# Optimization experiments

Measured on AMD Instinct MI355X. Metric: run time of the kernel, lower is better.

The kernel has to match this reference:

```python
import jax, jax.numpy as jnp
import numpy as np

INHIBITION = 3.0

def kwta(x, gates):
    # per-row k = argmax index of the gate row; keep the top-k values of x,
    # damp all other entries by 1/INHIBITION (matches torch loop + topk + scatter)
    k = jnp.argmax(gates, axis=1)                          # [B] int
    ranks = jnp.argsort(jnp.argsort(-x, axis=1), axis=1)   # rank 0 == largest
    keep = ranks < k[:, None]
    return jnp.where(keep, x, x / INHIBITION)

def _linear_init(key, out_d, in_d):
    k1, k2 = jax.random.split(key)
    lim = 1.0 / np.sqrt(in_d)
    W = jax.random.uniform(k1, (out_d, in_d), jnp.float32, -lim, lim)
    b = jax.random.uniform(k2, (out_d,), jnp.float32, -lim, lim)
    return W, b

def setup_inputs() -> dict:
    key = jax.random.key(0)
    B, S, H, HID = 16384, 512, 256, 512
    inp_dim = 2 * S + 4 + H  # 1284
    keys = jax.random.split(key, 13)
    d = {}
    d["state"] = jax.random.normal(keys[0], (B, 2 * S), jnp.float32)
    d["task_indicator"] = jax.random.normal(keys[1], (B, 4), jnp.float32)
    d["action"] = jax.random.normal(keys[2], (B, H), jnp.float32)
    specs = [("cx1_1", 2 * HID, inp_dim), ("cx1_2", 2 * HID, 2 * HID),
             ("cx2_1", HID, inp_dim), ("cx2_2", HID, HID),
             ("cx3_1", H, inp_dim), ("cx3_2", H, H),
             ("l1", 2 * HID, inp_dim), ("l2", HID, 2 * HID),
             ("l3", H, HID), ("l4", H, H)]
    for i, (name, o, idim) in enumerate(specs):
        W, b = _linear_init(keys[3 + i], o, idim)
        d["W_" + name] = W
        d["b_" + name] = b
    return d

def reference(state, task_indicator, action,
              W_cx1_1, b_cx1_1, W_cx1_2, b_cx1_2,
              W_cx2_1, b_cx2_1, W_cx2_2, b_cx2_2,
              W_cx3_1, b_cx3_1, W_cx3_2, b_cx3_2,
              W_l1, b_l1, W_l2, b_l2, W_l3, b_l3, W_l4, b_l4):
    ctx = jnp.concatenate([state, task_indicator, action], axis=1)  # [B, 1284]

    def gate(Wa, ba, Wb, bb):
        h = jnp.tanh(ctx @ Wa.T + ba)
        return jax.nn.softmax(h @ Wb.T + bb, axis=1)

    cx1 = gate(W_cx1_1, b_cx1_1, W_cx1_2, b_cx1_2)  # [B, 1024]
    cx2 = gate(W_cx2_1, b_cx2_1, W_cx2_2, b_cx2_2)  # [B, 512]
    cx3 = gate(W_cx3_1, b_cx3_1, W_cx3_2, b_cx3_2)  # [B, 256]

    x = kwta(ctx @ W_l1.T + b_l1, cx1)
    x = kwta(x @ W_l2.T + b_l2, cx2)
    x = kwta(x @ W_l3.T + b_l3, cx3)
    return x @ W_l4.T + b_l4  # [B, 256]
```

## Files before the change

kernel.cpp:

```cpp
#include <hip/hip_runtime.h>
#include <math.h>

typedef float  v4f   __attribute__((ext_vector_type(4)));
typedef double v2d   __attribute__((ext_vector_type(2)));
typedef double v4d   __attribute__((ext_vector_type(4)));
typedef float  f32x4 __attribute__((ext_vector_type(4)));
typedef short  s16x8 __attribute__((ext_vector_type(8)));

#define NB   16384
#define KCTX 1284
#define CSL  (KCTX/4)

#if defined(__has_builtin)
#  if __has_builtin(__builtin_amdgcn_mfma_f64_16x16x4f64)
#    define MFMA64(a, b, c) __builtin_amdgcn_mfma_f64_16x16x4f64((a), (b), (c), 0, 0, 0)
#  endif
#endif
#ifndef MFMA64
static __device__ __forceinline__ v4d mfma64_asm(double a, double b, v4d c) {
  asm volatile("v_mfma_f64_16x16x4_f64 %0, %1, %2, %0" : "+v"(c) : "v"(a), "v"(b));
  return c;
}
#  define MFMA64(a, b, c) mfma64_asm((a), (b), (c))
#endif

static __device__ __forceinline__ f32x4 mfma_bf16(s16x8 a, s16x8 b, f32x4 c) {
  asm volatile("v_mfma_f32_16x16x32_bf16 %0, %1, %2, %0" : "+v"(c) : "v"(a), "v"(b));
  return c;
}
#define MFMA_GUARD() do {                                  \
  __builtin_amdgcn_sched_barrier(0);                       \
  asm volatile("s_nop 7\ns_nop 7\ns_nop 7\ns_nop 7");      \
  __builtin_amdgcn_sched_barrier(0);                       \
} while (0)

__global__ __launch_bounds__(256) void k_build_ctx(
    const float* __restrict__ state, const float* __restrict__ task,
    const float* __restrict__ action, float* __restrict__ Cg)
{
  int idx = blockIdx.x * 256 + threadIdx.x;
  if (idx >= NB * CSL) return;
  int b = idx / CSL, s = idx - b * CSL;
  v4f v;
  if (s < 256)       v = *((const v4f*)state  + (size_t)b * 256 + s);
  else if (s == 256) v = *((const v4f*)task   + b);
  else               v = *((const v4f*)action + (size_t)b * 64 + (s - 257));
  *((v4f*)Cg + idx) = v;
}

__device__ __forceinline__ unsigned long long f64_ord(double f) {
  unsigned long long u = (unsigned long long)__double_as_longlong(f);
  return (u & 0x8000000000000000ull) ? ~u : (u | 0x8000000000000000ull);
}

__global__ __launch_bounds__(256) void k_split_w(
    const float* __restrict__ W, unsigned short* __restrict__ out,
    int N, int K, int KP)
{
  int idx = blockIdx.x * 256 + threadIdx.x;
  size_t total = (size_t)N * KP;
  if (idx >= (int)total) return;
  int n = idx / KP, k = idx - n * KP;
  float v = (k < K) ? W[(size_t)n * K + k] : 0.f;
  unsigned u1 = __float_as_uint(v);
  float f1 = __uint_as_float(u1 & 0xFFFF0000u);
  float r1 = v - f1;
  unsigned u2 = __float_as_uint(r1);
  float f2 = __uint_as_float(u2 & 0xFFFF0000u);
  float r2 = r1 - f2;
  out[idx]             = (unsigned short)(u1 >> 16);
  out[total + idx]     = (unsigned short)(u2 >> 16);
  out[2 * total + idx] = (unsigned short)(__float_as_uint(r2) >> 16);
}

#define TM 128
#define TN 64
#define TK 16
#define LRA 130
#define LRB 66

template<int EPI, int ASRC>
__global__ __launch_bounds__(256, 3) void g64m(
    const void* __restrict__ Av, const float* __restrict__ W,
    const float* __restrict__ bias, void* __restrict__ Cv,
    unsigned long long* __restrict__ kpk, int N, int K)
{
  __shared__ __align__(16) double As[TK * LRA];
  __shared__ __align__(16) double Ws[TK * LRB];

  const int tid  = threadIdx.x;
  const int lane = tid & 63;
  const int wid  = tid >> 6;
  const int wm   = wid >> 1;
  const int wn   = wid & 1;
  const int grp  = lane >> 4;
  const int lid  = lane & 15;
  const int row0 = blockIdx.x * TM;
  const int col0 = blockIdx.y * TN;

  const int lrA = tid >> 1;
  const int lcA = (tid & 1) * 8;
  const int lrW = tid >> 2;
  const int lcW = (tid & 3) * 4;

  const float*  ApF = (const float*)Av  + (size_t)(row0 + lrA) * K;
  const double* ApD = (const double*)Av + (size_t)(row0 + lrA) * K;
  const float*  WpF = W + (size_t)(col0 + lrW) * K;

  double sa[8], sw[4];

  v4d acc[4][2];
  #pragma unroll
  for (int i = 0; i < 4; ++i)
    #pragma unroll
    for (int j = 0; j < 2; ++j) { acc[i][j][0] = 0.0; acc[i][j][1] = 0.0;
                                  acc[i][j][2] = 0.0; acc[i][j][3] = 0.0; }

  const int nt = (K + TK - 1) / TK;

  auto loadA = [&](int k0) {
    const int kb = k0 + lcA;
    if (ASRC == 0) {
      if (kb + 8 <= K) {
        v4f x0 = *(const v4f*)(ApF + kb), x1 = *(const v4f*)(ApF + kb + 4);
        sa[0] = x0.x; sa[1] = x0.y; sa[2] = x0.z; sa[3] = x0.w;
        sa[4] = x1.x; sa[5] = x1.y; sa[6] = x1.z; sa[7] = x1.w;
      } else {
        #pragma unroll
        for (int j = 0; j < 8; ++j) sa[j] = (kb + j < K) ? (double)ApF[kb + j] : 0.0;
      }
    } else {
      const double* p = ApD + kb;
      v2d d0 = *(const v2d*)p,       d1 = *(const v2d*)(p + 2);
      v2d d2 = *(const v2d*)(p + 4), d3 = *(const v2d*)(p + 6);
      sa[0] = d0.x; sa[1] = d0.y; sa[2] = d1.x; sa[3] = d1.y;
      sa[4] = d2.x; sa[5] = d2.y; sa[6] = d3.x; sa[7] = d3.y;
    }
  };
  auto loadW = [&](int k0) {
    const int kb = k0 + lcW;
    if (kb + 4 <= K) {
      v4f w0 = *(const v4f*)(WpF + kb);
      sw[0] = w0.x; sw[1] = w0.y; sw[2] = w0.z; sw[3] = w0.w;
    } else {
      #pragma unroll
      for (int j = 0; j < 4; ++j) sw[j] = (kb + j < K) ? (double)WpF[kb + j] : 0.0;
    }
  };

  loadA(0); loadW(0);

  for (int t = 0; t < nt; ++t) {
    __syncthreads();
    #pragma unroll
    for (int j = 0; j < 8; ++j) As[(lcA + j) * LRA + lrA] = sa[j];
    #pragma unroll
    for (int j = 0; j < 4; ++j) Ws[(lcW + j) * LRB + lrW] = sw[j];
    if (t + 1 < nt) { loadA((t + 1) * TK); loadW((t + 1) * TK); }
    __syncthreads();
    #pragma unroll
    for (int ks = 0; ks < 4; ++ks) {
      const double* Ar = As + (ks * 4 + grp) * LRA + wm * 64 + lid;
      const double* Br = Ws + (ks * 4 + grp) * LRB + wn * 32 + lid;
      double a[4], b[2];
      #pragma unroll
      for (int i = 0; i < 4; ++i) a[i] = Ar[i * 16];
      #pragma unroll
      for (int j = 0; j < 2; ++j) b[j] = Br[j * 16];
      #pragma unroll
      for (int i = 0; i < 4; ++i)
        #pragma unroll
        for (int j = 0; j < 2; ++j)
          acc[i][j] = MFMA64(a[i], b[j], acc[i][j]);
    }
  }

  double bb[2];
  #pragma unroll
  for (int j = 0; j < 2; ++j) bb[j] = (double)bias[col0 + wn * 32 + j * 16 + lid];

  if (EPI == 0) {
    #pragma unroll
    for (int i = 0; i < 4; ++i)
      #pragma unroll
      for (int r = 0; r < 4; ++r) {
        int row = row0 + wm * 64 + i * 16 + r * 4 + grp;
        double* Cp = (double*)Cv + (size_t)row * N + col0 + wn * 32 + lid;
        #pragma unroll
        for (int j = 0; j < 2; ++j) Cp[j * 16] = acc[i][j][r] + bb[j];
      }
  } else if (EPI == 3 || EPI == 4) {
    #pragma unroll
    for (int i = 0; i < 4; ++i)
      #pragma unroll
      for (int r = 0; r < 4; ++r) {
        int row = row0 + wm * 64 + i * 16 + r * 4 + grp;
        float* Cp = (float*)Cv + (size_t)row * N + col0 + wn * 32 + lid;
        #pragma unroll
        for (int j = 0; j < 2; ++j) {
          double o = acc[i][j][r] + bb[j];
          if (EPI == 4) o = tanh(o);
          Cp[j * 16] = (float)o;
        }
      }
  } else {
    #pragma unroll
    for (int i = 0; i < 4; ++i)
      #pragma unroll
      for (int r = 0; r < 4; ++r) {
        int row = row0 + wm * 64 + i * 16 + r * 4 + grp;
        double best = acc[i][0][r] + bb[0];
        int bcol = col0 + wn * 32 + lid;
        {
          double v = acc[i][1][r] + bb[1];
          if (v > best) { best = v; bcol = col0 + wn * 32 + 16 + lid; }
        }
        #pragma unroll
        for (int d = 1; d < 16; d <<= 1) {
          double ov = __shfl_xor(best, d);
          int    oc = __shfl_xor(bcol, d);
          if (ov > best || (ov == best && oc < bcol)) { best = ov; bcol = oc; }
        }
        if (lid == 0) {
          unsigned long long key =
              (f64_ord(best) & ~0xFFFFull) | ((~(unsigned)bcol) & 0xFFFFu);
          atomicMax(&kpk[row], key);
        }
      }
  }
}

#define GTM 64
#define GTN 128
#define GTK 32
#define GLR 40

template<int EPI, int ASPLIT>
__global__ __launch_bounds__(256, 2) void g16(
    const void* __restrict__ Av, size_t aplane,
    const unsigned short* __restrict__ WS_,
    const float* __restrict__ bias,
    unsigned short* __restrict__ Hout, size_t hplane,
    unsigned long long* __restrict__ kpk, int N, int K, int KP)
{
  __shared__ __align__(16) unsigned short Al[3][GTM * GLR];
  __shared__ __align__(16) unsigned short Wl[3][GTN * GLR];

  const int tid  = threadIdx.x;
  const int lane = tid & 63;
  const int wid  = tid >> 6;
  const int grp  = lane >> 4;
  const int lid  = lane & 15;
  const int row0 = blockIdx.x * GTM;
  const int col0 = blockIdx.y * GTN;

  const int arow = tid >> 2, akc = (tid & 3) * 8;
  const int wrow = tid >> 1, wkc = (tid & 1) * 16;
  const float*          ApF = (const float*)Av + (size_t)(row0 + arow) * K;
  const unsigned short* ApS = (const unsigned short*)Av + (size_t)(row0 + arow) * K;
  const unsigned short* WpS = WS_ + (size_t)(col0 + wrow) * KP + wkc;
  const size_t wplane = (size_t)N * KP;

  float av[8];
  s16x8 sA[3], sW[3][2];

  f32x4 ah[4][2], am[4][2], al[4][2];
  double sh[4][2][4];
  #pragma unroll
  for (int i = 0; i < 4; ++i)
    #pragma unroll
    for (int j = 0; j < 2; ++j) {
      ah[i][j] = (f32x4)0.f; am[i][j] = (f32x4)0.f; al[i][j] = (f32x4)0.f;
      #pragma unroll
      for (int r = 0; r < 4; ++r) sh[i][j][r] = 0.0;
    }

  const int nt = KP / GTK;

  auto loadA = [&](int kb) {
    if (ASPLIT == 0) {
      #pragma unroll
      for (int q = 0; q < 2; ++q) {
        int k = kb + akc + q * 4;
        if (k + 4 <= K) {
          v4f x = *(const v4f*)(ApF + k);
          av[q*4+0] = x.x; av[q*4+1] = x.y; av[q*4+2] = x.z; av[q*4+3] = x.w;
        } else {
          #pragma unroll
          for (int j = 0; j < 4; ++j) av[q*4+j] = (k + j < K) ? ApF[k + j] : 0.f;
        }
      }
    } else {
      #pragma unroll
      for (int p = 0; p < 3; ++p)
        sA[p] = *(const s16x8*)(ApS + p * aplane + kb + akc);
    }
  };
  auto loadW = [&](int kb) {
    #pragma unroll
    for (int p = 0; p < 3; ++p) {
      const unsigned short* s = WpS + p * wplane + kb;
      sW[p][0] = *(const s16x8*)s;
      sW[p][1] = *(const s16x8*)(s + 8);
    }
  };

  auto split8 = [](const float* v, s16x8& p1, s16x8& p2, s16x8& p3) {
    #pragma unroll
    for (int j = 0; j < 8; ++j) {
      unsigned u1 = __float_as_uint(v[j]);
      float f1 = __uint_as_float(u1 & 0xFFFF0000u);
      float r1 = v[j] - f1;
      unsigned u2 = __float_as_uint(r1);
      float f2 = __uint_as_float(u2 & 0xFFFF0000u);
      float r2 = r1 - f2;
      p1[j] = (short)(u1 >> 16); p2[j] = (short)(u2 >> 16);
      p3[j] = (short)(__float_as_uint(r2) >> 16);
    }
  };

  loadA(0); loadW(0);

  for (int t = 0; t < nt; ++t) {
    __syncthreads();
    if (ASPLIT == 0) {
      s16x8 p1, p2, p3;
      split8(av, p1, p2, p3);
      *(s16x8*)&Al[0][arow * GLR + akc] = p1;
      *(s16x8*)&Al[1][arow * GLR + akc] = p2;
      *(s16x8*)&Al[2][arow * GLR + akc] = p3;
    } else {
      #pragma unroll
      for (int p = 0; p < 3; ++p)
        *(s16x8*)&Al[p][arow * GLR + akc] = sA[p];
    }
    #pragma unroll
    for (int p = 0; p < 3; ++p) {
      *(s16x8*)&Wl[p][wrow * GLR + wkc]     = sW[p][0];
      *(s16x8*)&Wl[p][wrow * GLR + wkc + 8] = sW[p][1];
    }
    if (t + 1 < nt) { loadA((t + 1) * GTK); loadW((t + 1) * GTK); }
    __syncthreads();

    s16x8 b0[2], b1[2], b2[2];
    #pragma unroll
    for (int nf = 0; nf < 2; ++nf) {
      int widx = (wid * 32 + nf * 16 + lid) * GLR + grp * 8;
      b0[nf] = *(const s16x8*)&Wl[0][widx];
      b1[nf] = *(const s16x8*)&Wl[1][widx];
      b2[nf] = *(const s16x8*)&Wl[2][widx];
    }
    #pragma unroll
    for (int mf = 0; mf < 4; ++mf) {
      int aidx = (mf * 16 + lid) * GLR + grp * 8;
      s16x8 a0 = *(const s16x8*)&Al[0][aidx];
      s16x8 a1 = *(const s16x8*)&Al[1][aidx];
      s16x8 a2 = *(const s16x8*)&Al[2][aidx];
      #pragma unroll
      for (int nf = 0; nf < 2; ++nf) {
        ah[mf][nf] = mfma_bf16(a0, b0[nf], ah[mf][nf]);
        am[mf][nf] = mfma_bf16(a0, b1[nf], am[mf][nf]);
        am[mf][nf] = mfma_bf16(a1, b0[nf], am[mf][nf]);
        al[mf][nf] = mfma_bf16(a0, b2[nf], al[mf][nf]);
        al[mf][nf] = mfma_bf16(a1, b1[nf], al[mf][nf]);
        al[mf][nf] = mfma_bf16(a2, b0[nf], al[mf][nf]);
      }
    }
    if ((t & 7) == 7) {
      MFMA_GUARD();
      #pragma unroll
      for (int mf = 0; mf < 4; ++mf)
        #pragma unroll
        for (int nf = 0; nf < 2; ++nf) {
          #pragma unroll
          for (int r = 0; r < 4; ++r) sh[mf][nf][r] += (double)ah[mf][nf][r];
          ah[mf][nf] = (f32x4)0.f;
        }
    }
  }

  MFMA_GUARD();
  #pragma unroll
  for (int mf = 0; mf < 4; ++mf)
    #pragma unroll
    for (int nf = 0; nf < 2; ++nf)
      #pragma unroll
      for (int r = 0; r < 4; ++r) sh[mf][nf][r] += (double)ah[mf][nf][r];

  double bb[2];
  #pragma unroll
  for (int nf = 0; nf < 2; ++nf) bb[nf] = (double)bias[col0 + wid * 32 + nf * 16 + lid];

  if (EPI == 4) {
    #pragma unroll
    for (int mf = 0; mf < 4; ++mf)
      #pragma unroll
      for (int r = 0; r < 4; ++r) {
        int row = row0 + mf * 16 + grp * 4 + r;
        float* Hp = (float*)Hout + (size_t)row * N + col0 + wid * 32 + lid;
        #pragma unroll
        for (int nf = 0; nf < 2; ++nf) {
          double o = sh[mf][nf][r] + (double)am[mf][nf][r] + (double)al[mf][nf][r] + bb[nf];
          Hp[nf * 16] = (float)tanh(o);
        }
      }
  } else {
    #pragma unroll
    for (int mf = 0; mf < 4; ++mf)
      #pragma unroll
      for (int r = 0; r < 4; ++r) {
        int row = row0 + mf * 16 + grp * 4 + r;
        double v0 = sh[mf][0][r] + (double)am[mf][0][r] + (double)al[mf][0][r] + bb[0];
        double v1 = sh[mf][1][r] + (double)am[mf][1][r] + (double)al[mf][1][r] + bb[1];
        double best = v0; int bcol = col0 + wid * 32 + lid;
        if (v1 > best) { best = v1; bcol = col0 + wid * 32 + 16 + lid; }
        #pragma unroll
        for (int d = 1; d < 16; d <<= 1) {
          double ov = __shfl_xor(best, d);
          int    oc = __shfl_xor(bcol, d);
          if (ov > best || (ov == best && oc < bcol)) { best = ov; bcol = oc; }
        }
        if (lid == 0) {
          unsigned long long key =
              (f64_ord(best) & ~0xFFFFull) | ((~(unsigned)bcol) & 0xFFFFu);
          atomicMax(&kpk[row], key);
        }
      }
  }
}

__global__ __launch_bounds__(256) void k_kwta64(
    double* __restrict__ X, int N, const unsigned long long* __restrict__ kpk)
{
  const int row = blockIdx.x;
  const int tid = threadIdx.x;
  const int lane = tid & 63;
  const int wv   = tid >> 6;
  double* x = X + (size_t)row * N;
  __shared__ unsigned long long su[1024];
  __shared__ int hist[256];
  __shared__ int wsum[4];
  __shared__ int s_bin, s_base, s_cnt;

  unsigned long long p = kpk[row];
  int k = (int)((~p) & 0xFFFFull);

  for (int j = tid; j < N; j += 256) su[j] = f64_ord(x[j]);
  __syncthreads();

  unsigned long long uth = 0xFFFFFFFFFFFFFFFFull;
  if (k > 0) {
    int t = N - k;
    unsigned long long prefix = 0;
    for (int shift = 56; shift >= 0; shift -= 8) {
      hist[tid] = 0;
      __syncthreads();
      unsigned long long pm =
          (shift == 56) ? 0ull : ~((1ull << (shift + 8)) - 1ull);
      for (int j = tid; j < N; j += 256) {
        unsigned long long u = su[j];
        if ((u & pm) == prefix) atomicAdd(&hist[(int)((u >> shift) & 255)], 1);
      }
      __syncthreads();
      int h = hist[tid];
      int xsc = h;
      #pragma unroll
      for (int d = 1; d < 64; d <<= 1) {
        int y = __shfl_up(xsc, d, 64);
        if (lane >= d) xsc += y;
      }
      if (lane == 63) wsum[wv] = xsc;
      __syncthreads();
      int add = 0;
      #pragma unroll
      for (int i = 0; i < 3; ++i) if (i < wv) add += wsum[i];
      int incl = xsc + add;
      int excl = incl - h;
      if (h > 0 && t >= excl && t < incl) {
        s_bin = tid; s_base = excl; s_cnt = h;
      }
      __syncthreads();
      prefix |= ((unsigned long long)s_bin) << shift;
      t -= s_base;
      int cnt = s_cnt;
      __syncthreads();
      if (cnt == 1) break;
    }
    uth = prefix;
  }
  __syncthreads();
  for (int j = tid; j < N; j += 256) {
    if (su[j] < uth) x[j] = x[j] / 3.0;
  }
}

extern "C" void kernel_launch(void* const* d_in, const int* in_sizes, int n_in,
                              void* d_out, int out_size, void* d_ws, size_t ws_size,
                              hipStream_t stream)
{
  const float* state   = (const float*)d_in[0];
  const float* task    = (const float*)d_in[1];
  const float* action  = (const float*)d_in[2];
  const float* W_cx1_1 = (const float*)d_in[3];  const float* b_cx1_1 = (const float*)d_in[4];
  const float* W_cx1_2 = (const float*)d_in[5];  const float* b_cx1_2 = (const float*)d_in[6];
  const float* W_cx2_1 = (const float*)d_in[7];  const float* b_cx2_1 = (const float*)d_in[8];
  const float* W_cx2_2 = (const float*)d_in[9];  const float* b_cx2_2 = (const float*)d_in[10];
  const float* W_cx3_1 = (const float*)d_in[11]; const float* b_cx3_1 = (const float*)d_in[12];
  const float* W_cx3_2 = (const float*)d_in[13]; const float* b_cx3_2 = (const float*)d_in[14];
  const float* W_l1    = (const float*)d_in[15]; const float* b_l1    = (const float*)d_in[16];
  const float* W_l2    = (const float*)d_in[17]; const float* b_l2    = (const float*)d_in[18];
  const float* W_l3    = (const float*)d_in[19]; const float* b_l3    = (const float*)d_in[20];
  const float* W_l4    = (const float*)d_in[21]; const float* b_l4    = (const float*)d_in[22];

  char* wsb = (char*)d_ws;
  double* A1 = (double*)wsb;
  float*  Hf = (float*)wsb;
  double* A3 = (double*)wsb;
  unsigned short* WS  = (unsigned short*)(wsb + 100663296ULL);
  float*  Cg = (float*)(wsb + 134217728ULL);
  double* A2 = (double*)(wsb + 134217728ULL);
  unsigned long long* kpk = (unsigned long long*)d_out;

  const size_t o_c11 = 0;
  const size_t o_c12 = 4030464;
  const size_t o_c21 = 7176192;
  const size_t o_c22 = 9191424;
  const size_t o_c31 = 9977856;
  const size_t o_c32 = 10985472;

  dim3 blk(256);

  k_build_ctx<<<(NB * CSL) / 256, blk, 0, stream>>>(state, task, action, Cg);
  (void)hipMemsetAsync(kpk, 0, (size_t)3 * NB * 8, stream);

  k_split_w<<<(1024*1312 + 255)/256, blk, 0, stream>>>(W_cx1_1, WS + o_c11, 1024, KCTX, 1312);
  k_split_w<<<(1024*1024 + 255)/256, blk, 0, stream>>>(W_cx1_2, WS + o_c12, 1024, 1024, 1024);
  k_split_w<<<( 512*1312 + 255)/256, blk, 0, stream>>>(W_cx2_1, WS + o_c21,  512, KCTX, 1312);
  k_split_w<<<( 512* 512 + 255)/256, blk, 0, stream>>>(W_cx2_2, WS + o_c22,  512,  512,  512);
  k_split_w<<<( 256*1312 + 255)/256, blk, 0, stream>>>(W_cx3_1, WS + o_c31,  256, KCTX, 1312);
  k_split_w<<<( 256* 256 + 255)/256, blk, 0, stream>>>(W_cx3_2, WS + o_c32,  256,  256,  256);

  g16<4,0><<<dim3(NB/GTM, 1024/GTN), blk, 0, stream>>>(Cg, 0, WS + o_c11, b_cx1_1,
      (unsigned short*)Hf, 0, nullptr, 1024, KCTX, 1312);
  g16<2,0><<<dim3(NB/GTM, 1024/GTN), blk, 0, stream>>>(Hf, 0, WS + o_c12, b_cx1_2,
      nullptr, 0, kpk, 1024, 1024, 1024);
  g16<4,0><<<dim3(NB/GTM,  512/GTN), blk, 0, stream>>>(Cg, 0, WS + o_c21, b_cx2_1,
      (unsigned short*)Hf, 0, nullptr, 512, KCTX, 1312);
  g16<2,0><<<dim3(NB/GTM,  512/GTN), blk, 0, stream>>>(Hf, 0, WS + o_c22, b_cx2_2,
      nullptr, 0, kpk + NB, 512, 512, 512);
  g16<4,0><<<dim3(NB/GTM,  256/GTN), blk, 0, stream>>>(Cg, 0, WS + o_c31, b_cx3_1,
      (unsigned short*)Hf, 0, nullptr, 256, KCTX, 1312);
  g16<2,0><<<dim3(NB/GTM,  256/GTN), blk, 0, stream>>>(Hf, 0, WS + o_c32, b_cx3_2,
      nullptr, 0, kpk + 2 * NB, 256, 256, 256);

  g64m<0,0><<<dim3(NB/TM, 1024/TN), blk, 0, stream>>>(Cg, W_l1, b_l1, A1, nullptr, 1024, KCTX);
  k_kwta64<<<NB, blk, 0, stream>>>(A1, 1024, kpk);
  g64m<0,1><<<dim3(NB/TM,  512/TN), blk, 0, stream>>>(A1, W_l2, b_l2, A2, nullptr,  512, 1024);
  k_kwta64<<<NB, blk, 0, stream>>>(A2,  512, kpk + NB);
  g64m<0,1><<<dim3(NB/TM,  256/TN), blk, 0, stream>>>(A2, W_l3, b_l3, A3, nullptr,  256,  512);
  k_kwta64<<<NB, blk, 0, stream>>>(A3,  256, kpk + 2*NB);
  g64m<3,1><<<dim3(NB/TM,  256/TN), blk, 0, stream>>>(A3, W_l4, b_l4, (float*)d_out, nullptr, 256, 256);
}
```

Before: 2.206 ms.

## Fuse prep kernels into one launch and double-buffer LDS in f64 GEMM

Merges context building, the six bf16 weight-split kernels and the kpk memset into a single k_prep launch, to cut launch overhead. The f64 MFMA GEMM now uses double-buffered shared memory: the next tile is staged into the alternate buffer after the MFMAs, leaving one barrier per iteration instead of two. This doubles LDS usage per block, which could reduce occupancy.

```diff
diff --git a/kernel.cpp b/kernel.cpp
--- a/kernel.cpp
+++ b/kernel.cpp
@@ -34,32 +34,25 @@
   __builtin_amdgcn_sched_barrier(0);                       \
 } while (0)
 
-__global__ __launch_bounds__(256) void k_build_ctx(
-    const float* __restrict__ state, const float* __restrict__ task,
-    const float* __restrict__ action, float* __restrict__ Cg)
-{
-  int idx = blockIdx.x * 256 + threadIdx.x;
-  if (idx >= NB * CSL) return;
-  int b = idx / CSL, s = idx - b * CSL;
-  v4f v;
-  if (s < 256)       v = *((const v4f*)state  + (size_t)b * 256 + s);
-  else if (s == 256) v = *((const v4f*)task   + b);
-  else               v = *((const v4f*)action + (size_t)b * 64 + (s - 257));
-  *((v4f*)Cg + idx) = v;
-}
-
 __device__ __forceinline__ unsigned long long f64_ord(double f) {
   unsigned long long u = (unsigned long long)__double_as_longlong(f);
   return (u & 0x8000000000000000ull) ? ~u : (u | 0x8000000000000000ull);
 }
 
-__global__ __launch_bounds__(256) void k_split_w(
+#define CT_ITEMS  (NB * CSL)
+#define E_C11     (1024 * 1312)
+#define E_C12     (1024 * 1024)
+#define E_C21     ( 512 * 1312)
+#define E_C22     ( 512 *  512)
+#define E_C31     ( 256 * 1312)
+#define E_C32     ( 256 *  256)
+#define KPK_ITEMS (3 * NB)
+
+static __device__ __forceinline__ void split_one(
     const float* __restrict__ W, unsigned short* __restrict__ out,
-    int N, int K, int KP)
+    int N, int K, int KP, int idx)
 {
-  int idx = blockIdx.x * 256 + threadIdx.x;
   size_t total = (size_t)N * KP;
-  if (idx >= (int)total) return;
   int n = idx / KP, k = idx - n * KP;
   float v = (k < K) ? W[(size_t)n * K + k] : 0.f;
   unsigned u1 = __float_as_uint(v);
@@ -73,6 +66,42 @@
   out[2 * total + idx] = (unsigned short)(__float_as_uint(r2) >> 16);
 }
 
+__global__ __launch_bounds__(256) void k_prep(
+    const float* __restrict__ state, const float* __restrict__ task,
+    const float* __restrict__ action, float* __restrict__ Cg,
+    const float* __restrict__ W1, const float* __restrict__ W2,
+    const float* __restrict__ W3, const float* __restrict__ W4,
+    const float* __restrict__ W5, const float* __restrict__ W6,
+    unsigned short* __restrict__ WS,
+    unsigned long long* __restrict__ kpk,
+    size_t o11, size_t o12, size_t o21, size_t o22, size_t o31, size_t o32)
+{
+  int idx = blockIdx.x * 256 + threadIdx.x;
+  if (idx < CT_ITEMS) {
+    int b = idx / CSL, s = idx - b * CSL;
+    v4f v;
+    if (s < 256)       v = *((const v4f*)state  + (size_t)b * 256 + s);
+    else if (s == 256) v = *((const v4f*)task   + b);
+    else               v = *((const v4f*)action + (size_t)b * 64 + (s - 257));
+    *((v4f*)Cg + idx) = v;
+    return;
+  }
+  idx -= CT_ITEMS;
+  if (idx < E_C11) { split_one(W1, WS + o11, 1024, KCTX, 1312, idx); return; }
+  idx -= E_C11;
+  if (idx < E_C12) { split_one(W2, WS + o12, 1024, 1024, 1024, idx); return; }
+  idx -= E_C12;
+  if (idx < E_C21) { split_one(W3, WS + o21,  512, KCTX, 1312, idx); return; }
+  idx -= E_C21;
+  if (idx < E_C22) { split_one(W4, WS + o22,  512,  512,  512, idx); return; }
+  idx -= E_C22;
+  if (idx < E_C31) { split_one(W5, WS + o31,  256, KCTX, 1312, idx); return; }
+  idx -= E_C31;
+  if (idx < E_C32) { split_one(W6, WS + o32,  256,  256,  256, idx); return; }
+  idx -= E_C32;
+  if (idx < KPK_ITEMS) kpk[idx] = 0ull;
+}
+
 #define TM 128
 #define TN 64
 #define TK 16
@@ -85,8 +114,8 @@
     const float* __restrict__ bias, void* __restrict__ Cv,
     unsigned long long* __restrict__ kpk, int N, int K)
 {
-  __shared__ __align__(16) double As[TK * LRA];
-  __shared__ __align__(16) double Ws[TK * LRB];
+  __shared__ __align__(16) double As[2][TK * LRA];
+  __shared__ __align__(16) double Ws[2][TK * LRB];
 
   const int tid  = threadIdx.x;
   const int lane = tid & 63;
@@ -147,21 +176,24 @@
       for (int j = 0; j < 4; ++j) sw[j] = (kb + j < K) ? (double)WpF[kb + j] : 0.0;
     }
   };
+  auto stage = [&](int buf) {
+    #pragma unroll
+    for (int j = 0; j < 8; ++j) As[buf][(lcA + j) * LRA + lrA] = sa[j];
+    #pragma unroll
+    for (int j = 0; j < 4; ++j) Ws[buf][(lcW + j) * LRB + lrW] = sw[j];
+  };
 
   loadA(0); loadW(0);
+  stage(0);
+  __syncthreads();
 
   for (int t = 0; t < nt; ++t) {
-    __syncthreads();
-    #pragma unroll
-    for (int j = 0; j < 8; ++j) As[(lcA + j) * LRA + lrA] = sa[j];
-    #pragma unroll
-    for (int j = 0; j < 4; ++j) Ws[(lcW + j) * LRB + lrW] = sw[j];
+    const int cb = t & 1;
     if (t + 1 < nt) { loadA((t + 1) * TK); loadW((t + 1) * TK); }
-    __syncthreads();
     #pragma unroll
     for (int ks = 0; ks < 4; ++ks) {
-      const double* Ar = As + (ks * 4 + grp) * LRA + wm * 64 + lid;
-      const double* Br = Ws + (ks * 4 + grp) * LRB + wn * 32 + lid;
+      const double* Ar = As[cb] + (ks * 4 + grp) * LRA + wm * 64 + lid;
+      const double* Br = Ws[cb] + (ks * 4 + grp) * LRB + wn * 32 + lid;
       double a[4], b[2];
       #pragma unroll
       for (int i = 0; i < 4; ++i) a[i] = Ar[i * 16];
@@ -173,6 +205,8 @@
         for (int j = 0; j < 2; ++j)
           acc[i][j] = MFMA64(a[i], b[j], acc[i][j]);
     }
+    if (t + 1 < nt) stage(cb ^ 1);
+    __syncthreads();
   }
 
   double bb[2];
@@ -530,15 +564,10 @@
 
   dim3 blk(256);
 
-  k_build_ctx<<<(NB * CSL) / 256, blk, 0, stream>>>(state, task, action, Cg);
-  (void)hipMemsetAsync(kpk, 0, (size_t)3 * NB * 8, stream);
-
-  k_split_w<<<(1024*1312 + 255)/256, blk, 0, stream>>>(W_cx1_1, WS + o_c11, 1024, KCTX, 1312);
-  k_split_w<<<(1024*1024 + 255)/256, blk, 0, stream>>>(W_cx1_2, WS + o_c12, 1024, 1024, 1024);
-  k_split_w<<<( 512*1312 + 255)/256, blk, 0, stream>>>(W_cx2_1, WS + o_c21,  512, KCTX, 1312);
-  k_split_w<<<( 512* 512 + 255)/256, blk, 0, stream>>>(W_cx2_2, WS + o_c22,  512,  512,  512);
-  k_split_w<<<( 256*1312 + 255)/256, blk, 0, stream>>>(W_cx3_1, WS + o_c31,  256, KCTX, 1312);
-  k_split_w<<<( 256* 256 + 255)/256, blk, 0, stream>>>(W_cx3_2, WS + o_c32,  256,  256,  256);
+  k_prep<<<(CT_ITEMS + E_C11 + E_C12 + E_C21 + E_C22 + E_C31 + E_C32 + KPK_ITEMS) / 256,
+           blk, 0, stream>>>(state, task, action, Cg,
+                             W_cx1_1, W_cx1_2, W_cx2_1, W_cx2_2, W_cx3_1, W_cx3_2,
+                             WS, kpk, o_c11, o_c12, o_c21, o_c22, o_c31, o_c32);
 
   g16<4,0><<<dim3(NB/GTM, 1024/GTN), blk, 0, stream>>>(Cg, 0, WS + o_c11, b_cx1_1,
       (unsigned short*)Hf, 0, nullptr, 1024, KCTX, 1312);
```

After: 2.355 ms. 1.07x slower.
